# Kernel optimization log

Hardware: AMD Instinct MI355X
Metric: run time of the kernel (lower is better)

The kernel has to match this reference:

```python
import jax, jax.numpy as jnp
import numpy as np

STRIDE = 1
PADDING = 1


def _ternarize(w):
    # threshold = 0.75 * mean(|w|); alpha = mean(|w| over |w| > threshold)
    abs_w = jnp.abs(w)
    threshold = 0.75 * jnp.mean(abs_w)
    mask = abs_w > threshold
    cnt = jnp.sum(mask)
    alpha = jnp.where(cnt > 0, jnp.sum(jnp.where(mask, abs_w, 0.0)) / jnp.maximum(cnt, 1), 1.0)
    tern = jnp.where(w > threshold, alpha, jnp.where(w < -threshold, -alpha, 0.0))
    # straight-through estimator: forward uses tern, grad flows to w as identity
    return w + jax.lax.stop_gradient(tern - w)


def setup_inputs() -> dict:
    key = jax.random.key(0)
    k_x, k_w = jax.random.split(key)
    x = jax.random.normal(k_x, (32, 256, 56, 56), dtype=jnp.float32)
    weight = jax.random.normal(k_w, (256, 256, 3, 3), dtype=jnp.float32)
    return {"x": x, "weight": weight}


def reference(x, weight):
    tw = _ternarize(weight)
    # NCHW input, OIHW kernel
    return jax.lax.conv_general_dilated(
        x, tw,
        window_strides=(STRIDE, STRIDE),
        padding=[(PADDING, PADDING), (PADDING, PADDING)],
        dimension_numbers=("NCHW", "OIHW", "NCHW"),
    )
```

## Files before the change

kernel.cpp:

```cpp
#include <hip/hip_runtime.h>
#include <hip/hip_bf16.h>

typedef short short8 __attribute__((ext_vector_type(8)));
typedef float f32x4 __attribute__((ext_vector_type(4)));

constexpr int N_  = 32;
constexpr int C_  = 256;
constexpr int K_  = 256;
constexpr int H_  = 56;
constexpr int W_  = 56;
constexpr int HW_ = H_ * W_;
constexpr int NW_ = K_ * C_ * 9;

constexpr int TH   = 4;
constexpr int NB   = 14;
constexpr int HR   = 6, HC = 58;
constexpr int NH   = HR * HC;
constexpr int BROW = 80;
constexpr int BSZ  = NH * BROW;
constexpr int LDSB = 4 * BSZ;
constexpr int NPAIR2 = 8 * NH;
constexpr int SITER  = 6;
constexpr int ASTEP  = 16384;

constexpr int NQB   = 1152;
constexpr int WS_P1 = 4;
constexpr int WS_P2 = 300;
constexpr int WS_P3 = 1500;
constexpr size_t WS_WQ = 16384;
constexpr size_t WS_NEEDED = WS_WQ + (size_t)NW_ * 2;

__device__ __forceinline__ unsigned f2bf(float f) {
    unsigned u = __builtin_bit_cast(unsigned, f);
    return (u + 0x7FFFu + ((u >> 16) & 1u)) >> 16;
}

__global__ void k_abs_partial(const float* __restrict__ w, float* __restrict__ ws) {
    __shared__ float sm[4];
    float s = 0.f;
    for (int i = blockIdx.x * 256 + threadIdx.x; i < NW_; i += 256 * 256)
        s += fabsf(w[i]);
    #pragma unroll
    for (int o = 32; o > 0; o >>= 1) s += __shfl_down(s, o, 64);
    const int wid = threadIdx.x >> 6, lane = threadIdx.x & 63;
    if (lane == 0) sm[wid] = s;
    __syncthreads();
    if (threadIdx.x == 0) {
        float r = 0.f;
        for (int i = 0; i < 4; ++i) r += sm[i];
        ws[WS_P1 + blockIdx.x] = r;
    }
}

__device__ __forceinline__ float reduce256_all(const float* __restrict__ p, float* sm) {
    float v = threadIdx.x < 256 ? p[threadIdx.x] : 0.f;
    #pragma unroll
    for (int o = 32; o > 0; o >>= 1) v += __shfl_down(v, o, 64);
    const int wid = threadIdx.x >> 6, lane = threadIdx.x & 63;
    __syncthreads();
    if (lane == 0) sm[wid] = v;
    __syncthreads();
    float total = 0.f;
    #pragma unroll
    for (int i = 0; i < 8; ++i) total += sm[i];
    return total;
}

__global__ __launch_bounds__(512) void k_quant(const float* __restrict__ w,
                                               float* __restrict__ ws,
                                               unsigned short* __restrict__ wq) {
    __shared__ float sm[8];
    const float total = reduce256_all(ws + WS_P1, sm);
    const float thr = 0.75f * total / (float)NW_;
    const int i = blockIdx.x * 512 + threadIdx.x;
    const float v = w[i];
    const unsigned short q = v > thr ? (unsigned short)0x3F80
                                     : (v < -thr ? (unsigned short)0xBF80 : (unsigned short)0);
    const int k   = i / 2304;
    const int rem = i - k * 2304;
    const int c   = rem / 9;
    const int rs  = rem - c * 9;
    const int chi = c >> 5, c5 = c & 31;
    wq[(size_t)(chi * 9 + rs) * 8192 + (k << 5) + c5] = q;
    const float a = fabsf(v);
    float s = a > thr ? a : 0.f;
    float cn = a > thr ? 1.f : 0.f;
    #pragma unroll
    for (int o = 32; o > 0; o >>= 1) { s += __shfl_down(s, o, 64); cn += __shfl_down(cn, o, 64); }
    __shared__ float sm2[16];
    const int wid = threadIdx.x >> 6, lane = threadIdx.x & 63;
    __syncthreads();
    if (lane == 0) { sm2[wid] = s; sm2[8 + wid] = cn; }
    __syncthreads();
    if (threadIdx.x == 0) {
        float S = 0.f, C2 = 0.f;
        for (int j = 0; j < 8; ++j) { S += sm2[j]; C2 += sm2[8 + j]; }
        ws[WS_P2 + blockIdx.x] = S;
        ws[WS_P3 + blockIdx.x] = C2;
    }
}

__global__ void k_fb_total(float* __restrict__ ws) {
    __shared__ float sm[4];
    float v = ws[WS_P1 + threadIdx.x];
    #pragma unroll
    for (int o = 32; o > 0; o >>= 1) v += __shfl_down(v, o, 64);
    const int wid = threadIdx.x >> 6, lane = threadIdx.x & 63;
    if (lane == 0) sm[wid] = v;
    __syncthreads();
    if (threadIdx.x == 0) {
        float r = 0.f;
        for (int i = 0; i < 4; ++i) r += sm[i];
        ws[0] = r;
    }
}

__global__ void k_fb_masked(const float* __restrict__ w, float* __restrict__ ws) {
    const float thr = 0.75f * ws[0] / (float)NW_;
    float s = 0.f, c = 0.f;
    for (int i = blockIdx.x * 256 + threadIdx.x; i < NW_; i += 256 * 256) {
        float a = fabsf(w[i]);
        if (a > thr) { s += a; c += 1.f; }
    }
    #pragma unroll
    for (int o = 32; o > 0; o >>= 1) { s += __shfl_down(s, o, 64); c += __shfl_down(c, o, 64); }
    __shared__ float sm[8];
    const int wid = threadIdx.x >> 6, lane = threadIdx.x & 63;
    if (lane == 0) { sm[wid] = s; sm[4 + wid] = c; }
    __syncthreads();
    if (threadIdx.x == 0) {
        float S = 0.f, C2 = 0.f;
        for (int i = 0; i < 4; ++i) { S += sm[i]; C2 += sm[i + 4]; }
        ws[WS_P2 + blockIdx.x] = S;
        ws[WS_P3 + blockIdx.x] = C2;
    }
}

__global__ void k_final_masked(float* __restrict__ ws) {
    __shared__ float sm[8];
    float s = ws[WS_P2 + threadIdx.x];
    float c = ws[WS_P3 + threadIdx.x];
    #pragma unroll
    for (int o = 32; o > 0; o >>= 1) { s += __shfl_down(s, o, 64); c += __shfl_down(c, o, 64); }
    const int wid = threadIdx.x >> 6, lane = threadIdx.x & 63;
    if (lane == 0) { sm[wid] = s; sm[4 + wid] = c; }
    __syncthreads();
    if (threadIdx.x == 0) {
        float S = 0.f, C2 = 0.f;
        for (int i = 0; i < 4; ++i) { S += sm[i]; C2 += sm[i + 4]; }
        ws[1] = S; ws[2] = C2;
    }
}

constexpr int RSO_[9] = {
    (0*HC+0)*BROW, (0*HC+1)*BROW, (0*HC+2)*BROW,
    (1*HC+0)*BROW, (1*HC+1)*BROW, (1*HC+2)*BROW,
    (2*HC+0)*BROW, (2*HC+1)*BROW, (2*HC+2)*BROW };

struct ConvState {
    const float* xn;
    const char*  wqc;
    char*        ldsp;
    size_t       aoff;
    int          tid;
    int          bB[7];
    int          xrel[SITER];
    unsigned     okm;
};

__device__ __forceinline__ void load_a(short8 (&d)[4], const ConvState& st, int step) {
    const char* ap = st.wqc + (size_t)step * ASTEP + st.aoff;
    d[0] = *(const short8*)(ap);
    d[1] = *(const short8*)(ap + 1024);
    d[2] = *(const short8*)(ap + 2048);
    d[3] = *(const short8*)(ap + 3072);
}

__device__ __forceinline__ void issue_b(const ConvState& st, int c0, float (&bs)[SITER][4]) {
    #pragma unroll
    for (int it = 0; it < SITER; ++it) {
        const float* p = st.xn + (size_t)c0 * HW_ + st.xrel[it];
        bs[it][0] = p[0];
        bs[it][1] = p[HW_];
        bs[it][2] = p[2 * HW_];
        bs[it][3] = p[3 * HW_];
    }
}

__device__ __forceinline__ void write_b(const ConvState& st, int base,
                                        const float (&bs)[SITER][4]) {
    #pragma unroll
    for (int it = 0; it < SITER; ++it) {
        const int u = it * 512 + st.tid;
        if (u < NPAIR2) {
            const int c4 = u / NH, hidx = u - c4 * NH;
            const bool ok = (st.okm >> it) & 1u;
            const float f0 = ok ? bs[it][0] : 0.f;
            const float f1 = ok ? bs[it][1] : 0.f;
            const float f2 = ok ? bs[it][2] : 0.f;
            const float f3 = ok ? bs[it][3] : 0.f;
            uint2 v;
            v.x = f2bf(f0) | (f2bf(f1) << 16);
            v.y = f2bf(f2) | (f2bf(f3) << 16);
            *(uint2*)(st.ldsp + base + hidx * BROW + c4 * 8) = v;
        }
    }
}

template <int BUF, bool STAGE, bool BAR>
__device__ __forceinline__ void do_chunk(int chi, const ConvState& st,
                                         short8 (&afr)[2][4], f32x4 (&acc)[4][7],
                                         float (&bs)[SITER][4]) {
    constexpr int PAR    = BUF & 1;
    constexpr int rdbase = BUF * BSZ;
    constexpr int wrbase = ((BUF + 2) & 3) * BSZ;
    constexpr bool LASTCH = (BUF == 3) && !STAGE && !BAR;
    #pragma unroll
    for (int rs = 0; rs < 9; ++rs) {
        const int cur = (PAR + rs) & 1, nxt = cur ^ 1;
        const int step = chi * 9 + rs;
        if (!(LASTCH && rs == 8))
            load_a(afr[nxt], st, step + 1);

        short8 bfr[7];
        #pragma unroll
        for (int nf = 0; nf < 7; ++nf)
            bfr[nf] = *(const short8*)(st.ldsp + rdbase + st.bB[nf] + RSO_[rs]);

        if (STAGE && rs == 6)
            issue_b(st, (chi + 2) * 32, bs);

        __builtin_amdgcn_s_setprio(1);
        #pragma unroll
        for (int nf = 0; nf < 7; ++nf)
            #pragma unroll
            for (int mf = 0; mf < 4; ++mf)
                acc[mf][nf] = __builtin_amdgcn_mfma_f32_16x16x32_bf16(
                    afr[cur][mf], bfr[nf], acc[mf][nf], 0, 0, 0);
        __builtin_amdgcn_s_setprio(0);

        if (rs == 8) {
            if (STAGE) write_b(st, wrbase, bs);
            if (BAR) {
                asm volatile("s_waitcnt lgkmcnt(0)" ::: "memory");
                __builtin_amdgcn_s_barrier();
            }
        }
    }
}

__global__ __launch_bounds__(512, 2) void conv_mfma(const float* __restrict__ x,
                                                    const unsigned short* __restrict__ wq,
                                                    const float* __restrict__ wsc,
                                                    float* __restrict__ out) {
    extern __shared__ char lds[];
    const int tid = threadIdx.x, lane = tid & 63, wid = tid >> 6;
    const int wm = wid & 3, wn = wid >> 2, lr = lane & 15, lg = lane >> 4;
    const int band = blockIdx.x, n = blockIdx.y;
    const int h0 = band * TH;

    ConvState st;
    st.xn   = x + (size_t)n * C_ * HW_;
    st.wqc  = (const char*)wq;
    st.ldsp = lds;
    st.aoff = (size_t)(wm * 64 + lr) * 64 + lg * 16;
    st.tid  = tid;
    #pragma unroll
    for (int nf = 0; nf < 7; ++nf) {
        const int pos = wn * 112 + nf * 16 + lr;
        const int y = pos / 56, xx = pos - y * 56;
        st.bB[nf] = (y * HC + xx) * BROW + lg * 16;
    }
    st.okm = 0;
    #pragma unroll
    for (int it = 0; it < SITER; ++it) {
        const int u  = it * 512 + tid;
        const bool vu = u < NPAIR2;
        const int uu = vu ? u : 0;
        const int c4 = uu / NH, hidx = uu - c4 * NH;
        const int hy = hidx / HC, hx = hidx - hy * HC;
        const int h = h0 - 1 + hy, w = hx - 1;
        const bool ok = vu && (unsigned)h < (unsigned)H_ && (unsigned)w < (unsigned)W_;
        st.xrel[it] = ok ? (4 * c4 * HW_ + h * W_ + w) : 0;
        st.okm |= (ok ? 1u : 0u) << it;
    }

    f32x4 acc[4][7] = {};
    short8 afr[2][4];
    float bs[SITER][4];

    load_a(afr[0], st, 0);
    issue_b(st, 0, bs);
    write_b(st, 0 * BSZ, bs);
    issue_b(st, 32, bs);
    write_b(st, 1 * BSZ, bs);
    asm volatile("s_waitcnt lgkmcnt(0)" ::: "memory");
    __builtin_amdgcn_s_barrier();

    do_chunk<0, true,  false>(0, st, afr, acc, bs);
    do_chunk<1, true,  true >(1, st, afr, acc, bs);
    do_chunk<2, true,  false>(2, st, afr, acc, bs);
    do_chunk<3, true,  true >(3, st, afr, acc, bs);
    do_chunk<0, true,  false>(4, st, afr, acc, bs);
    do_chunk<1, true,  true >(5, st, afr, acc, bs);
    do_chunk<2, false, false>(6, st, afr, acc, bs);
    do_chunk<3, false, false>(7, st, afr, acc, bs);

    __syncthreads();
    float* sred = (float*)lds;
    float s2 = wsc[WS_P2 + tid] + wsc[WS_P2 + 512 + tid];
    float s3 = wsc[WS_P3 + tid] + wsc[WS_P3 + 512 + tid];
    if (tid < NQB - 1024) {
        s2 += wsc[WS_P2 + 1024 + tid];
        s3 += wsc[WS_P3 + 1024 + tid];
    }
    #pragma unroll
    for (int o = 32; o > 0; o >>= 1) { s2 += __shfl_down(s2, o, 64); s3 += __shfl_down(s3, o, 64); }
    if (lane == 0) { sred[wid] = s2; sred[8 + wid] = s3; }
    __syncthreads();
    float msum = 0.f, mcnt = 0.f;
    #pragma unroll
    for (int i = 0; i < 8; ++i) { msum += sred[i]; mcnt += sred[8 + i]; }
    const float alpha = mcnt > 0.f ? msum / fmaxf(mcnt, 1.f) : 1.0f;

    #pragma unroll
    for (int mf = 0; mf < 4; ++mf) {
        const int k = wm * 64 + mf * 16 + lg * 4;
        #pragma unroll
        for (int nf = 0; nf < 7; ++nf) {
            const int pos = wn * 112 + nf * 16 + lr;
            const int y = pos / 56, xx = pos - y * 56;
            float* po = out + ((size_t)n * K_ + k) * HW_ + (h0 + y) * W_ + xx;
            #pragma unroll
            for (int j = 0; j < 4; ++j)
                po[(size_t)j * HW_] = alpha * acc[mf][nf][j];
        }
    }
}

constexpr int W4_ = W_ / 4;
constexpr int SP_ = H_ * W4_;
__global__ __launch_bounds__(256) void conv_tern_otf(const float* __restrict__ x,
                                                     const float* __restrict__ wt,
                                                     const float* __restrict__ wsc,
                                                     float* __restrict__ out) {
    const int kg = blockIdx.x, n = blockIdx.y, k0 = kg * 4;
    const float thr = 0.75f * wsc[0] / (float)NW_;
    const float cnt = wsc[2];
    const float alpha = cnt > 0.f ? wsc[1] / fmaxf(cnt, 1.f) : 1.0f;
    for (int j = 0; j < 4; ++j) {
        const int sp = (int)threadIdx.x + j * 256;
        if (sp >= SP_) break;
        const int h = sp / W4_, w0 = (sp % W4_) * 4;
        float acc[4][4];
        #pragma unroll
        for (int kt = 0; kt < 4; ++kt)
            #pragma unroll
            for (int jj = 0; jj < 4; ++jj) acc[kt][jj] = 0.f;
        for (int c = 0; c < C_; ++c) {
            const float* xp = x + (((size_t)n * C_ + c) * H_) * W_;
            float xr[3][6];
            #pragma unroll
            for (int r = 0; r < 3; ++r) {
                const int hh = h + r - 1;
                const float* rowp = xp + hh * W_;
                if ((unsigned)hh < (unsigned)H_) {
                    const float4 mid = *(const float4*)(rowp + w0);
                    xr[r][1] = mid.x; xr[r][2] = mid.y; xr[r][3] = mid.z; xr[r][4] = mid.w;
                    xr[r][0] = (w0 > 0)      ? rowp[w0 - 1] : 0.f;
                    xr[r][5] = (w0 + 4 < W_) ? rowp[w0 + 4] : 0.f;
                } else {
                    #pragma unroll
                    for (int q = 0; q < 6; ++q) xr[r][q] = 0.f;
                }
            }
            #pragma unroll
            for (int kt = 0; kt < 4; ++kt) {
                const float* wp = wt + ((size_t)(k0 + kt) * C_ + c) * 9;
                #pragma unroll
                for (int r = 0; r < 3; ++r)
                    #pragma unroll
                    for (int s = 0; s < 3; ++s) {
                        float wv = wp[r * 3 + s];
                        wv = wv > thr ? alpha : (wv < -thr ? -alpha : 0.f);
                        #pragma unroll
                        for (int jj = 0; jj < 4; ++jj)
                            acc[kt][jj] = fmaf(wv, xr[r][jj + s], acc[kt][jj]);
                    }
            }
        }
        #pragma unroll
        for (int kt = 0; kt < 4; ++kt) {
            float4 o;
            o.x = acc[kt][0]; o.y = acc[kt][1]; o.z = acc[kt][2]; o.w = acc[kt][3];
            *(float4*)(out + ((((size_t)n * K_ + (k0 + kt)) * H_ + h) * W_ + w0)) = o;
        }
    }
}

extern "C" void kernel_launch(void* const* d_in, const int* in_sizes, int n_in,
                              void* d_out, int out_size, void* d_ws, size_t ws_size,
                              hipStream_t stream) {
    const float* x = (const float*)d_in[0];
    const float* w = (const float*)d_in[1];
    float* out = (float*)d_out;
    float* ws  = (float*)d_ws;
    unsigned short* wq = (unsigned short*)((char*)d_ws + WS_WQ);

    k_abs_partial<<<256, 256, 0, stream>>>(w, ws);

    if (ws_size >= WS_NEEDED) {
        k_quant<<<NQB, 512, 0, stream>>>(w, ws, wq);
        hipFuncSetAttribute((const void*)conv_mfma,
                            hipFuncAttributeMaxDynamicSharedMemorySize, LDSB);
        dim3 grid(NB, N_);
        conv_mfma<<<grid, 512, LDSB, stream>>>(x, wq, ws, out);
    } else {
        k_fb_total<<<1, 256, 0, stream>>>(ws);
        k_fb_masked<<<256, 256, 0, stream>>>(w, ws);
        k_final_masked<<<1, 256, 0, stream>>>(ws);
        dim3 grid(64, N_);
        conv_tern_otf<<<grid, 256, 0, stream>>>(x, w, ws, out);
    }
}
```

Before: 144.0 us.

## Switch conv input staging from four-buffer to double-buffered LDS pipeline

Replaces the four-slot LDS ring, which prefetched two chunks ahead with a barrier every other chunk, by a two-slot double buffer that prefetches one chunk ahead and synchronises after every chunk. LDS becomes a static allocation of half the size, and the per-thread gather offsets are recomputed at each issue instead of being held in registers. The aim is lower LDS and register use, which may allow more blocks per CU. The cost is twice as many barriers and less slack to hide the global loads behind compute.

After: 128.3 us (median of 2 runs). -10.9%, faster.

```diff
diff --git a/kernel.cpp b/kernel.cpp
--- a/kernel.cpp
+++ b/kernel.cpp
@@ -18,7 +18,6 @@
 constexpr int NH   = HR * HC;
 constexpr int BROW = 80;
 constexpr int BSZ  = NH * BROW;
-constexpr int LDSB = 4 * BSZ;
 constexpr int NPAIR2 = 8 * NH;
 constexpr int SITER  = 6;
 constexpr int ASTEP  = 16384;
@@ -162,10 +161,8 @@
     const char*  wqc;
     char*        ldsp;
     size_t       aoff;
-    int          tid;
+    int          h0, tid;
     int          bB[7];
-    int          xrel[SITER];
-    unsigned     okm;
 };
 
 __device__ __forceinline__ void load_a(short8 (&d)[4], const ConvState& st, int step) {
@@ -176,25 +173,36 @@
     d[3] = *(const short8*)(ap + 3072);
 }
 
-__device__ __forceinline__ void issue_b(const ConvState& st, int c0, float (&bs)[SITER][4]) {
+__device__ __forceinline__ void issue_b(const ConvState& st, int c0,
+                                        float (&bs)[SITER][4], unsigned& bmask) {
+    bmask = 0;
     #pragma unroll
     for (int it = 0; it < SITER; ++it) {
-        const float* p = st.xn + (size_t)c0 * HW_ + st.xrel[it];
+        const int u  = it * 512 + st.tid;
+        const bool vu = u < NPAIR2;
+        const int uu = vu ? u : 0;
+        const int c4 = uu / NH, hidx = uu - c4 * NH;
+        const int hy = hidx / HC, hx = hidx - hy * HC;
+        const int h  = st.h0 - 1 + hy, w = hx - 1;
+        const bool ok = vu && (unsigned)h < (unsigned)H_ && (unsigned)w < (unsigned)W_;
+        const int off = ok ? ((c0 + 4 * c4) * HW_ + h * W_ + w) : 0;
+        const float* p = st.xn + off;
         bs[it][0] = p[0];
         bs[it][1] = p[HW_];
         bs[it][2] = p[2 * HW_];
         bs[it][3] = p[3 * HW_];
+        bmask |= (ok ? 1u : 0u) << it;
     }
 }
 
 __device__ __forceinline__ void write_b(const ConvState& st, int base,
-                                        const float (&bs)[SITER][4]) {
+                                        const float (&bs)[SITER][4], unsigned bmask) {
     #pragma unroll
     for (int it = 0; it < SITER; ++it) {
         const int u = it * 512 + st.tid;
         if (u < NPAIR2) {
             const int c4 = u / NH, hidx = u - c4 * NH;
-            const bool ok = (st.okm >> it) & 1u;
+            const bool ok = (bmask >> it) & 1u;
             const float f0 = ok ? bs[it][0] : 0.f;
             const float f1 = ok ? bs[it][1] : 0.f;
             const float f2 = ok ? bs[it][2] : 0.f;
@@ -207,14 +215,11 @@
     }
 }
 
-template <int BUF, bool STAGE, bool BAR>
+template <int PAR, bool LASTCH>
 __device__ __forceinline__ void do_chunk(int chi, const ConvState& st,
                                          short8 (&afr)[2][4], f32x4 (&acc)[4][7],
-                                         float (&bs)[SITER][4]) {
-    constexpr int PAR    = BUF & 1;
-    constexpr int rdbase = BUF * BSZ;
-    constexpr int wrbase = ((BUF + 2) & 3) * BSZ;
-    constexpr bool LASTCH = (BUF == 3) && !STAGE && !BAR;
+                                         float (&bs)[SITER][4], unsigned& bmask) {
+    const int rdbase = PAR * BSZ;
     #pragma unroll
     for (int rs = 0; rs < 9; ++rs) {
         const int cur = (PAR + rs) & 1, nxt = cur ^ 1;
@@ -226,9 +231,6 @@
         #pragma unroll
         for (int nf = 0; nf < 7; ++nf)
             bfr[nf] = *(const short8*)(st.ldsp + rdbase + st.bB[nf] + RSO_[rs]);
-
-        if (STAGE && rs == 6)
-            issue_b(st, (chi + 2) * 32, bs);
 
         __builtin_amdgcn_s_setprio(1);
         #pragma unroll
@@ -239,12 +241,12 @@
                     afr[cur][mf], bfr[nf], acc[mf][nf], 0, 0, 0);
         __builtin_amdgcn_s_setprio(0);
 
-        if (rs == 8) {
-            if (STAGE) write_b(st, wrbase, bs);
-            if (BAR) {
-                asm volatile("s_waitcnt lgkmcnt(0)" ::: "memory");
-                __builtin_amdgcn_s_barrier();
-            }
+        if (rs == 6 && !LASTCH)
+            issue_b(st, (chi + 1) * 32, bs, bmask);
+        if (rs == 8 && !LASTCH) {
+            write_b(st, (PAR ^ 1) * BSZ, bs, bmask);
+            asm volatile("s_waitcnt lgkmcnt(0)" ::: "memory");
+            __builtin_amdgcn_s_barrier();
         }
     }
 }
@@ -253,17 +255,17 @@
                                                     const unsigned short* __restrict__ wq,
                                                     const float* __restrict__ wsc,
                                                     float* __restrict__ out) {
-    extern __shared__ char lds[];
+    __shared__ char lds[2 * BSZ];
     const int tid = threadIdx.x, lane = tid & 63, wid = tid >> 6;
     const int wm = wid & 3, wn = wid >> 2, lr = lane & 15, lg = lane >> 4;
     const int band = blockIdx.x, n = blockIdx.y;
-    const int h0 = band * TH;
 
     ConvState st;
     st.xn   = x + (size_t)n * C_ * HW_;
     st.wqc  = (const char*)wq;
     st.ldsp = lds;
     st.aoff = (size_t)(wm * 64 + lr) * 64 + lg * 16;
+    st.h0   = band * TH;
     st.tid  = tid;
     #pragma unroll
     for (int nf = 0; nf < 7; ++nf) {
@@ -271,40 +273,24 @@
         const int y = pos / 56, xx = pos - y * 56;
         st.bB[nf] = (y * HC + xx) * BROW + lg * 16;
     }
-    st.okm = 0;
-    #pragma unroll
-    for (int it = 0; it < SITER; ++it) {
-        const int u  = it * 512 + tid;
-        const bool vu = u < NPAIR2;
-        const int uu = vu ? u : 0;
-        const int c4 = uu / NH, hidx = uu - c4 * NH;
-        const int hy = hidx / HC, hx = hidx - hy * HC;
-        const int h = h0 - 1 + hy, w = hx - 1;
-        const bool ok = vu && (unsigned)h < (unsigned)H_ && (unsigned)w < (unsigned)W_;
-        st.xrel[it] = ok ? (4 * c4 * HW_ + h * W_ + w) : 0;
-        st.okm |= (ok ? 1u : 0u) << it;
-    }
 
     f32x4 acc[4][7] = {};
     short8 afr[2][4];
     float bs[SITER][4];
-
+    unsigned bmask;
+
+    issue_b(st, 0, bs, bmask);
     load_a(afr[0], st, 0);
-    issue_b(st, 0, bs);
-    write_b(st, 0 * BSZ, bs);
-    issue_b(st, 32, bs);
-    write_b(st, 1 * BSZ, bs);
+    write_b(st, 0, bs, bmask);
     asm volatile("s_waitcnt lgkmcnt(0)" ::: "memory");
     __builtin_amdgcn_s_barrier();
 
-    do_chunk<0, true,  false>(0, st, afr, acc, bs);
-    do_chunk<1, true,  true >(1, st, afr, acc, bs);
-    do_chunk<2, true,  false>(2, st, afr, acc, bs);
-    do_chunk<3, true,  true >(3, st, afr, acc, bs);
-    do_chunk<0, true,  false>(4, st, afr, acc, bs);
-    do_chunk<1, true,  true >(5, st, afr, acc, bs);
-    do_chunk<2, false, false>(6, st, afr, acc, bs);
-    do_chunk<3, false, false>(7, st, afr, acc, bs);
+    for (int cc = 0; cc < 3; ++cc) {
+        do_chunk<0, false>(2 * cc,     st, afr, acc, bs, bmask);
+        do_chunk<1, false>(2 * cc + 1, st, afr, acc, bs, bmask);
+    }
+    do_chunk<0, false>(6, st, afr, acc, bs, bmask);
+    do_chunk<1, true >(7, st, afr, acc, bs, bmask);
 
     __syncthreads();
     float* sred = (float*)lds;
@@ -330,7 +316,7 @@
         for (int nf = 0; nf < 7; ++nf) {
             const int pos = wn * 112 + nf * 16 + lr;
             const int y = pos / 56, xx = pos - y * 56;
-            float* po = out + ((size_t)n * K_ + k) * HW_ + (h0 + y) * W_ + xx;
+            float* po = out + ((size_t)n * K_ + k) * HW_ + (st.h0 + y) * W_ + xx;
             #pragma unroll
             for (int j = 0; j < 4; ++j)
                 po[(size_t)j * HW_] = alpha * acc[mf][nf][j];
@@ -411,10 +397,8 @@
 
     if (ws_size >= WS_NEEDED) {
         k_quant<<<NQB, 512, 0, stream>>>(w, ws, wq);
-        hipFuncSetAttribute((const void*)conv_mfma,
-                            hipFuncAttributeMaxDynamicSharedMemorySize, LDSB);
         dim3 grid(NB, N_);
-        conv_mfma<<<grid, 512, LDSB, stream>>>(x, wq, ws, out);
+        conv_mfma<<<grid, 512, 0, stream>>>(x, wq, ws, out);
     } else {
         k_fb_total<<<1, 256, 0, stream>>>(ws);
         k_fb_masked<<<256, 256, 0, stream>>>(w, ws);
```
